# Kernel optimization log

Measured on AMD Instinct MI355X. Metric: run time of the kernel, lower is better.

Reference implementation:

```python
import jax, jax.numpy as jnp
import numpy as np

NUM_CLASSES = 80  # COCO
BATCH = 32
CH = 3 * (5 + NUM_CLASSES)  # 255
THRESH = 0.6


def _decode_scale(out, anchors, t, thresh):
    """Dense YOLO decode for one scale.
    out: [B, 3*(5+C), H, W]; anchors: [3, 2]; t: stride.
    Returns boxes [B*H*W*3, 6] and valid mask [B*H*W*3].
    """
    B, Ch, H, W = out.shape
    v = jnp.transpose(out, (0, 2, 3, 1)).reshape(B, H, W, 3, -1)  # [B,H,W,3,5+C]
    conf = jax.nn.sigmoid(v[..., 0])
    valid = conf > thresh  # objectness mask (compaction mask in torch version)
    gx = jnp.arange(W, dtype=v.dtype)[None, None, :, None]  # idxs[:,2]
    gy = jnp.arange(H, dtype=v.dtype)[None, :, None, None]  # idxs[:,1]
    cx = (gx + jax.nn.sigmoid(v[..., 1])) * t
    cy = (gy + jax.nn.sigmoid(v[..., 2])) * t
    w = anchors[:, 0] * jnp.exp(v[..., 3])  # anchor dim broadcasts over [B,H,W,3]
    h = anchors[:, 1] * jnp.exp(v[..., 4])
    x1 = cx - w * 0.5
    y1 = cy - h * 0.5
    x2 = x1 + w
    y2 = y1 + h
    cls = jnp.argmax(v[..., 5:], axis=-1).astype(v.dtype)
    boxes = jnp.stack([conf, x1, y1, x2, y2, cls], axis=-1).reshape(-1, 6)
    return boxes, valid.reshape(-1)


def setup_inputs() -> dict:
    key = jax.random.key(0)
    k13, k26, k52 = jax.random.split(key, 3)
    output_13 = jax.random.normal(k13, (BATCH, CH, 13, 13), jnp.float32)
    output_26 = jax.random.normal(k26, (BATCH, CH, 26, 26), jnp.float32)
    output_52 = jax.random.normal(k52, (BATCH, CH, 52, 52), jnp.float32)
    # standard YOLOv3 COCO anchors per scale
    anchors_13 = jnp.array([[116., 90.], [156., 198.], [373., 326.]], jnp.float32)
    anchors_26 = jnp.array([[30., 61.], [62., 45.], [59., 119.]], jnp.float32)
    anchors_52 = jnp.array([[10., 13.], [16., 30.], [33., 23.]], jnp.float32)
    thresh = jnp.float32(THRESH)
    return {"output_13": output_13, "output_26": output_26, "output_52": output_52,
            "anchors_13": anchors_13, "anchors_26": anchors_26, "anchors_52": anchors_52,
            "thresh": thresh}


def reference(output_13, output_26, output_52, anchors_13, anchors_26, anchors_52, thresh):
    b13, m13 = _decode_scale(output_13, anchors_13, 32.0, thresh)
    b26, m26 = _decode_scale(output_26, anchors_26, 16.0, thresh)
    b52, m52 = _decode_scale(output_52, anchors_52, 8.0, thresh)
    boxes = jnp.concatenate([b13, b26, b52], axis=0)
    valid = jnp.concatenate([m13, m26, m52], axis=0)
    # boxes[valid] equals the torch module's concatenated output rows
    return boxes, valid
```

## Files before the change

### kernel.cpp

```cpp
#include <hip/hip_runtime.h>


constexpr int BATCH = 32;
constexpr int NCLS  = 80;
constexpr int HW13  = 13 * 13;
constexpr int HW26  = 26 * 26;
constexpr int HW52  = 52 * 52;
constexpr int N13   = BATCH * 3 * HW13;
constexpr int N26   = BATCH * 3 * HW26;
constexpr int N52   = BATCH * 3 * HW52;
constexpr int NTOT  = N13 + N26 + N52;

template <int HW, int W>
__device__ __forceinline__ void decode_one(
    const float* __restrict__ in, const float* __restrict__ anc,
    float t, int li, int rowofs, float th,
    float* __restrict__ boxes, float* __restrict__ valid)
{
    const int hw   = li % HW;
    const int rest = li / HW;
    const int a    = rest % 3;
    const int b    = rest / 3;
    const int x    = hw % W;
    const int y    = hw / W;

    const float* p = in + (size_t)(b * 255 + a * 85) * HW + hw;

    const float t0 = p[0];
    const float t1 = p[(size_t)1 * HW];
    const float t2 = p[(size_t)2 * HW];
    const float t3 = p[(size_t)3 * HW];
    const float t4 = p[(size_t)4 * HW];

    float best = p[(size_t)5 * HW];
    int cls = 0;
    for (int k = 1; k < NCLS; ++k) {
        const float v = p[(size_t)(5 + k) * HW];
        if (v > best) { best = v; cls = k; }
    }

    const float conf = 1.0f / (1.0f + expf(-t0));
    const float cx   = ((float)x + 1.0f / (1.0f + expf(-t1))) * t;
    const float cy   = ((float)y + 1.0f / (1.0f + expf(-t2))) * t;
    const float w    = anc[a * 2 + 0] * expf(t3);
    const float h    = anc[a * 2 + 1] * expf(t4);
    const float x1   = cx - w * 0.5f;
    const float y1   = cy - h * 0.5f;
    const float x2   = x1 + w;
    const float y2   = y1 + h;

    const int row = rowofs + (b * HW + hw) * 3 + a;
    float* o = boxes + (size_t)row * 6;
    o[0] = conf; o[1] = x1; o[2] = y1; o[3] = x2; o[4] = y2; o[5] = (float)cls;
    valid[row] = conf > th ? 1.0f : 0.0f;
}

__global__ __launch_bounds__(256) void yolo_decode_kernel(
    const float* __restrict__ in13, const float* __restrict__ in26,
    const float* __restrict__ in52,
    const float* __restrict__ a13, const float* __restrict__ a26,
    const float* __restrict__ a52,
    const float* __restrict__ pth, float* __restrict__ out)
{
    const int i = blockIdx.x * blockDim.x + threadIdx.x;
    if (i >= NTOT) return;
    const float th = *pth;
    float* boxes = out;
    float* valid = out + (size_t)NTOT * 6;

    if (i < N13) {
        decode_one<HW13, 13>(in13, a13, 32.0f, i, 0, th, boxes, valid);
    } else if (i < N13 + N26) {
        decode_one<HW26, 26>(in26, a26, 16.0f, i - N13, N13, th, boxes, valid);
    } else {
        decode_one<HW52, 52>(in52, a52, 8.0f, i - (N13 + N26), N13 + N26, th, boxes, valid);
    }
}

extern "C" void kernel_launch(void* const* d_in, const int* in_sizes, int n_in,
                              void* d_out, int out_size, void* d_ws, size_t ws_size,
                              hipStream_t stream) {
    const float* in13 = (const float*)d_in[0];
    const float* in26 = (const float*)d_in[1];
    const float* in52 = (const float*)d_in[2];
    const float* a13  = (const float*)d_in[3];
    const float* a26  = (const float*)d_in[4];
    const float* a52  = (const float*)d_in[5];
    const float* pth  = (const float*)d_in[6];
    float* out = (float*)d_out;

    const int block = 256;
    const int grid  = (NTOT + block - 1) / block;
    yolo_decode_kernel<<<grid, block, 0, stream>>>(in13, in26, in52,
                                                   a13, a26, a52, pth, out);
}
```

Measured before the change: 32.40 us.

## Vectorize channel loads with float4 and remap threads to anchor-by-position blocks

Each thread in the 26 and 52 scales now processes four adjacent spatial positions, loading each channel as a float4, and the 13 scale keeps scalar loads. Blocks of 192 threads map one wavefront to each anchor, replacing the flat index decode with per-block batch and chunk indexing. The class argmax loop is unrolled and made branchless with fmaxf and selects. This is meant to reduce load instruction count and improve memory-level parallelism on a bandwidth-bound read of about 80 channels. The cost is more registers per thread and stores to the output rows that are less contiguous.

Measured after the change: 28.89 us. 10.8% less time.

```diff
diff --git a/kernel.cpp b/kernel.cpp
--- a/kernel.cpp
+++ b/kernel.cpp
@@ -1,29 +1,37 @@
 #include <hip/hip_runtime.h>
 
 
+constexpr int NCLS  = 80;
 constexpr int BATCH = 32;
-constexpr int NCLS  = 80;
-constexpr int HW13  = 13 * 13;
-constexpr int HW26  = 26 * 26;
-constexpr int HW52  = 52 * 52;
+constexpr int HW13  = 169;
+constexpr int HW26  = 676;
+constexpr int HW52  = 2704;
 constexpr int N13   = BATCH * 3 * HW13;
 constexpr int N26   = BATCH * 3 * HW26;
 constexpr int N52   = BATCH * 3 * HW52;
 constexpr int NTOT  = N13 + N26 + N52;
+constexpr int R13   = 0;
+constexpr int R26   = N13;
+constexpr int R52   = N13 + N26;
+
+constexpr int OUT13 = (HW13 + 63) / 64;
+constexpr int OUT26 = (HW26 / 4 + 63) / 64;
+constexpr int OUT52 = (HW52 / 4 + 63) / 64;
+constexpr int B13   = BATCH * OUT13;
+constexpr int B26   = BATCH * OUT26;
+constexpr int B52   = BATCH * OUT52;
+constexpr int NBLK  = B13 + B26 + B52;
+
+__device__ __forceinline__ float sigm(float x) { return 1.0f / (1.0f + expf(-x)); }
 
 template <int HW, int W>
-__device__ __forceinline__ void decode_one(
+__device__ __forceinline__ void decode_scalar(
     const float* __restrict__ in, const float* __restrict__ anc,
-    float t, int li, int rowofs, float th,
+    float t, int b, int a, int hw, int rowofs, float th,
     float* __restrict__ boxes, float* __restrict__ valid)
 {
-    const int hw   = li % HW;
-    const int rest = li / HW;
-    const int a    = rest % 3;
-    const int b    = rest / 3;
-    const int x    = hw % W;
-    const int y    = hw / W;
-
+    const int x = hw % W;
+    const int y = hw / W;
     const float* p = in + (size_t)(b * 255 + a * 85) * HW + hw;
 
     const float t0 = p[0];
@@ -34,46 +42,118 @@
 
     float best = p[(size_t)5 * HW];
     int cls = 0;
+#pragma unroll
     for (int k = 1; k < NCLS; ++k) {
         const float v = p[(size_t)(5 + k) * HW];
-        if (v > best) { best = v; cls = k; }
+        cls  = v > best ? k : cls;
+        best = fmaxf(v, best);
     }
 
-    const float conf = 1.0f / (1.0f + expf(-t0));
-    const float cx   = ((float)x + 1.0f / (1.0f + expf(-t1))) * t;
-    const float cy   = ((float)y + 1.0f / (1.0f + expf(-t2))) * t;
-    const float w    = anc[a * 2 + 0] * expf(t3);
-    const float h    = anc[a * 2 + 1] * expf(t4);
+    const float aw = anc[a * 2 + 0], ah = anc[a * 2 + 1];
+    const float conf = sigm(t0);
+    const float cx   = ((float)x + sigm(t1)) * t;
+    const float cy   = ((float)y + sigm(t2)) * t;
+    const float w    = aw * expf(t3);
+    const float h    = ah * expf(t4);
     const float x1   = cx - w * 0.5f;
     const float y1   = cy - h * 0.5f;
-    const float x2   = x1 + w;
-    const float y2   = y1 + h;
 
     const int row = rowofs + (b * HW + hw) * 3 + a;
     float* o = boxes + (size_t)row * 6;
-    o[0] = conf; o[1] = x1; o[2] = y1; o[3] = x2; o[4] = y2; o[5] = (float)cls;
+    o[0] = conf; o[1] = x1; o[2] = y1; o[3] = x1 + w; o[4] = y1 + h; o[5] = (float)cls;
     valid[row] = conf > th ? 1.0f : 0.0f;
 }
 
-__global__ __launch_bounds__(256) void yolo_decode_kernel(
+template <int HW, int W>
+__device__ __forceinline__ void decode_vec4(
+    const float* __restrict__ in, const float* __restrict__ anc,
+    float t, int b, int a, int c, int rowofs, float th,
+    float* __restrict__ boxes, float* __restrict__ valid)
+{
+    constexpr int HWc = HW / 4;
+    const float4* __restrict__ p =
+        reinterpret_cast<const float4*>(in + (size_t)(b * 255 + a * 85) * HW) + c;
+
+    const float4 t0 = p[0];
+    const float4 t1 = p[(size_t)1 * HWc];
+    const float4 t2 = p[(size_t)2 * HWc];
+    const float4 t3 = p[(size_t)3 * HWc];
+    const float4 t4 = p[(size_t)4 * HWc];
+
+    float4 bv = p[(size_t)5 * HWc];
+    float b0 = bv.x, b1 = bv.y, b2 = bv.z, b3 = bv.w;
+    int c0 = 0, c1 = 0, c2 = 0, c3 = 0;
+#pragma unroll
+    for (int k = 1; k < NCLS; ++k) {
+        const float4 v = p[(size_t)(5 + k) * HWc];
+        c0 = v.x > b0 ? k : c0;  b0 = fmaxf(v.x, b0);
+        c1 = v.y > b1 ? k : c1;  b1 = fmaxf(v.y, b1);
+        c2 = v.z > b2 ? k : c2;  b2 = fmaxf(v.z, b2);
+        c3 = v.w > b3 ? k : c3;  b3 = fmaxf(v.w, b3);
+    }
+
+    const float aw = anc[a * 2 + 0], ah = anc[a * 2 + 1];
+
+#define EMIT(j, s0, s1, s2, s3, s4, cc)                                   \
+    {                                                                     \
+        const int hw = 4 * c + (j);                                       \
+        const int x = hw % W;                                             \
+        const int y = hw / W;                                             \
+        const float conf = sigm(s0);                                      \
+        const float cx = ((float)x + sigm(s1)) * t;                       \
+        const float cy = ((float)y + sigm(s2)) * t;                       \
+        const float w_ = aw * expf(s3);                                   \
+        const float h_ = ah * expf(s4);                                   \
+        const float x1 = cx - w_ * 0.5f;                                  \
+        const float y1 = cy - h_ * 0.5f;                                  \
+        const int row = rowofs + (b * HW + hw) * 3 + a;                   \
+        float* o = boxes + (size_t)row * 6;                               \
+        o[0] = conf; o[1] = x1; o[2] = y1;                                \
+        o[3] = x1 + w_; o[4] = y1 + h_; o[5] = (float)(cc);               \
+        valid[row] = conf > th ? 1.0f : 0.0f;                             \
+    }
+
+    EMIT(0, t0.x, t1.x, t2.x, t3.x, t4.x, c0);
+    EMIT(1, t0.y, t1.y, t2.y, t3.y, t4.y, c1);
+    EMIT(2, t0.z, t1.z, t2.z, t3.z, t4.z, c2);
+    EMIT(3, t0.w, t1.w, t2.w, t3.w, t4.w, c3);
+#undef EMIT
+}
+
+__global__ __launch_bounds__(192) void yolo_decode_kernel(
     const float* __restrict__ in13, const float* __restrict__ in26,
     const float* __restrict__ in52,
     const float* __restrict__ a13, const float* __restrict__ a26,
     const float* __restrict__ a52,
     const float* __restrict__ pth, float* __restrict__ out)
 {
-    const int i = blockIdx.x * blockDim.x + threadIdx.x;
-    if (i >= NTOT) return;
+    const int a    = threadIdx.x >> 6;
+    const int lane = threadIdx.x & 63;
     const float th = *pth;
     float* boxes = out;
     float* valid = out + (size_t)NTOT * 6;
 
-    if (i < N13) {
-        decode_one<HW13, 13>(in13, a13, 32.0f, i, 0, th, boxes, valid);
-    } else if (i < N13 + N26) {
-        decode_one<HW26, 26>(in26, a26, 16.0f, i - N13, N13, th, boxes, valid);
+    int blk = blockIdx.x;
+    if (blk < B13) {
+        const int b  = blk / OUT13;
+        const int co = blk % OUT13;
+        const int hw = co * 64 + lane;
+        if (hw >= HW13) return;
+        decode_scalar<HW13, 13>(in13, a13, 32.0f, b, a, hw, R13, th, boxes, valid);
+    } else if (blk < B13 + B26) {
+        blk -= B13;
+        const int b  = blk / OUT26;
+        const int co = blk % OUT26;
+        const int c  = co * 64 + lane;
+        if (c >= HW26 / 4) return;
+        decode_vec4<HW26, 26>(in26, a26, 16.0f, b, a, c, R26, th, boxes, valid);
     } else {
-        decode_one<HW52, 52>(in52, a52, 8.0f, i - (N13 + N26), N13 + N26, th, boxes, valid);
+        blk -= (B13 + B26);
+        const int b  = blk / OUT52;
+        const int co = blk % OUT52;
+        const int c  = co * 64 + lane;
+        if (c >= HW52 / 4) return;
+        decode_vec4<HW52, 52>(in52, a52, 8.0f, b, a, c, R52, th, boxes, valid);
     }
 }
 
@@ -89,8 +169,6 @@
     const float* pth  = (const float*)d_in[6];
     float* out = (float*)d_out;
 
-    const int block = 256;
-    const int grid  = (NTOT + block - 1) / block;
-    yolo_decode_kernel<<<grid, block, 0, stream>>>(in13, in26, in52,
-                                                   a13, a26, a52, pth, out);
+    yolo_decode_kernel<<<NBLK, 192, 0, stream>>>(in13, in26, in52,
+                                                 a13, a26, a52, pth, out);
 }
```

## Remap threads to output rows, unroll class argmax, vectorize box stores

Applied to the files above, without the earlier changes.

Reorders the thread-to-work mapping so consecutive threads handle consecutive output rows (anchor index fastest) instead of consecutive spatial positions. The 80-class argmax loop is unrolled in groups of 16 loads with branchless selects to raise memory-level parallelism. Box outputs are written with float2 stores. The remapping makes output writes contiguous but spreads each wavefront's input reads across three anchor planes, which may reduce read coalescing on the dominant input traffic.

New measurement: 37.73 us. +16.4%, slower.

```diff
diff --git a/kernel.cpp b/kernel.cpp
--- a/kernel.cpp
+++ b/kernel.cpp
@@ -1,28 +1,30 @@
 #include <hip/hip_runtime.h>
 
 
+constexpr int NCLS  = 80;
 constexpr int BATCH = 32;
-constexpr int NCLS  = 80;
-constexpr int HW13  = 13 * 13;
-constexpr int HW26  = 26 * 26;
-constexpr int HW52  = 52 * 52;
+constexpr int HW13  = 169;
+constexpr int HW26  = 676;
+constexpr int HW52  = 2704;
 constexpr int N13   = BATCH * 3 * HW13;
 constexpr int N26   = BATCH * 3 * HW26;
 constexpr int N52   = BATCH * 3 * HW52;
 constexpr int NTOT  = N13 + N26 + N52;
 
+__device__ __forceinline__ float sigm(float x) { return 1.0f / (1.0f + expf(-x)); }
+
 template <int HW, int W>
-__device__ __forceinline__ void decode_one(
+__device__ __forceinline__ void decode_row(
     const float* __restrict__ in, const float* __restrict__ anc,
-    float t, int li, int rowofs, float th,
+    float t, int li, int row, float th,
     float* __restrict__ boxes, float* __restrict__ valid)
 {
-    const int hw   = li % HW;
-    const int rest = li / HW;
-    const int a    = rest % 3;
-    const int b    = rest / 3;
-    const int x    = hw % W;
-    const int y    = hw / W;
+    const int a   = li % 3;
+    const int pos = li / 3;
+    const int hw  = pos % HW;
+    const int b   = pos / HW;
+    const int x   = hw % W;
+    const int y   = hw / W;
 
     const float* p = in + (size_t)(b * 255 + a * 85) * HW + hw;
 
@@ -33,25 +35,35 @@
     const float t4 = p[(size_t)4 * HW];
 
     float best = p[(size_t)5 * HW];
-    int cls = 0;
-    for (int k = 1; k < NCLS; ++k) {
-        const float v = p[(size_t)(5 + k) * HW];
-        if (v > best) { best = v; cls = k; }
+    int   cls  = 0;
+
+#pragma unroll
+    for (int k0 = 1; k0 < NCLS; k0 += 16) {
+        float v[16];
+#pragma unroll
+        for (int j = 0; j < 16; ++j)
+            if (k0 + j < NCLS) v[j] = p[(size_t)(5 + k0 + j) * HW];
+#pragma unroll
+        for (int j = 0; j < 16; ++j)
+            if (k0 + j < NCLS) {
+                cls  = v[j] > best ? (k0 + j) : cls;
+                best = fmaxf(v[j], best);
+            }
     }
 
-    const float conf = 1.0f / (1.0f + expf(-t0));
-    const float cx   = ((float)x + 1.0f / (1.0f + expf(-t1))) * t;
-    const float cy   = ((float)y + 1.0f / (1.0f + expf(-t2))) * t;
-    const float w    = anc[a * 2 + 0] * expf(t3);
-    const float h    = anc[a * 2 + 1] * expf(t4);
+    const float aw = anc[a * 2 + 0], ah = anc[a * 2 + 1];
+    const float conf = sigm(t0);
+    const float cx   = ((float)x + sigm(t1)) * t;
+    const float cy   = ((float)y + sigm(t2)) * t;
+    const float w    = aw * expf(t3);
+    const float h    = ah * expf(t4);
     const float x1   = cx - w * 0.5f;
     const float y1   = cy - h * 0.5f;
-    const float x2   = x1 + w;
-    const float y2   = y1 + h;
 
-    const int row = rowofs + (b * HW + hw) * 3 + a;
-    float* o = boxes + (size_t)row * 6;
-    o[0] = conf; o[1] = x1; o[2] = y1; o[3] = x2; o[4] = y2; o[5] = (float)cls;
+    float2* o = reinterpret_cast<float2*>(boxes + (size_t)row * 6);
+    o[0] = make_float2(conf, x1);
+    o[1] = make_float2(y1, x1 + w);
+    o[2] = make_float2(y1 + h, (float)cls);
     valid[row] = conf > th ? 1.0f : 0.0f;
 }
 
@@ -69,11 +81,11 @@
     float* valid = out + (size_t)NTOT * 6;
 
     if (i < N13) {
-        decode_one<HW13, 13>(in13, a13, 32.0f, i, 0, th, boxes, valid);
+        decode_row<HW13, 13>(in13, a13, 32.0f, i, i, th, boxes, valid);
     } else if (i < N13 + N26) {
-        decode_one<HW26, 26>(in26, a26, 16.0f, i - N13, N13, th, boxes, valid);
+        decode_row<HW26, 26>(in26, a26, 16.0f, i - N13, i, th, boxes, valid);
     } else {
-        decode_one<HW52, 52>(in52, a52, 8.0f, i - (N13 + N26), N13 + N26, th, boxes, valid);
+        decode_row<HW52, 52>(in52, a52, 8.0f, i - (N13 + N26), i, th, boxes, valid);
     }
 }
 
```
